# Kernel optimization log

Measured on AMD Instinct MI355X. Metric: run time of the kernel, lower is better.

Reference implementation:

```python
import jax, jax.numpy as jnp
import numpy as np

B, T, D, H = 2, 2048, 2048, 16
DK = D // H  # 128
THETA = 10000.0


def _rope_angles():
    inv_freq = 1.0 / (THETA ** (np.arange(0, DK, 2, dtype=np.float32) / DK))  # (DK/2,)
    pos = np.arange(T, dtype=np.float32)
    freqs = pos[:, None] * inv_freq[None, :]  # (T, DK/2)
    return jnp.asarray(np.broadcast_to(freqs[None], (B, T, DK // 2)).copy())


def setup_inputs() -> dict:
    key = jax.random.key(0)
    k1, k2, k3 = jax.random.split(key, 3)
    x = jax.random.normal(k1, (B, T, D), dtype=jnp.float32)
    Wqkv = jax.random.normal(k2, (D, 3 * D), dtype=jnp.float32) * (D ** -0.5)
    Wout = jax.random.normal(k3, (D, D), dtype=jnp.float32) * (D ** -0.5)
    return {"x": x, "freqs": _rope_angles(), "Wqkv": Wqkv, "Wout": Wout}


def _apply_rope(xh, cos, sin):
    # xh: (B,T,H,DK); consecutive pairs form complex numbers (torch view_as_complex)
    xr = xh[..., 0::2]  # (B,T,H,DK/2) real parts
    xi = xh[..., 1::2]  # imag parts
    # cos/sin: (B,T,1,DK/2)
    or_ = xr * cos - xi * sin
    oi_ = xr * sin + xi * cos
    return jnp.stack([or_, oi_], axis=-1).reshape(xh.shape)


def reference(x, freqs, Wqkv, Wout):
    qkv = x @ Wqkv  # (B,T,3D)
    qkv = qkv.reshape(B, T, H, 3 * DK)
    q, k, v = qkv[..., :DK], qkv[..., DK:2 * DK], qkv[..., 2 * DK:]
    cos = jnp.cos(freqs)[:, :, None, :]
    sin = jnp.sin(freqs)[:, :, None, :]
    q = _apply_rope(q, cos, sin)
    k = _apply_rope(k, cos, sin)
    # (B,H,T,DK)
    q = q.transpose(0, 2, 1, 3)
    k = k.transpose(0, 2, 1, 3)
    v = v.transpose(0, 2, 1, 3)
    scores = jnp.einsum('bhqd,bhkd->bhqk', q, k) * (DK ** -0.5)
    causal = jnp.tril(jnp.ones((T, T), dtype=bool))
    scores = jnp.where(causal[None, None], scores, -jnp.inf)
    attn = jax.nn.softmax(scores, axis=-1)
    attn = jnp.nan_to_num(attn)
    out = jnp.einsum('bhqk,bhkd->bhqd', attn, v)  # (B,H,T,DK)
    out = out.transpose(0, 2, 1, 3).reshape(B, T, D)
    return out @ Wout
```

## Files before the change

### kernel.cpp

```cpp
#include <hip/hip_runtime.h>
#include <cstdint>

#define BATCH   2
#define T_SEQ   2048
#define NH      16
#define DK      128
#define DMODEL  2048
#define NQKV    6144

using short8 = __attribute__((ext_vector_type(8))) short;
using f32x4  = __attribute__((ext_vector_type(4))) float;
using f32x16 = __attribute__((ext_vector_type(16))) float;

__device__ __forceinline__ float bf2f(unsigned short u) {
    union { float f; uint32_t i; } x; x.i = ((uint32_t)u) << 16; return x.f;
}
__device__ __forceinline__ unsigned short f2bf(float f) {
    union { float f; uint32_t i; } x; x.f = f;
    uint32_t r = x.i + 0x7fffu + ((x.i >> 16) & 1u);
    return (unsigned short)(r >> 16);
}

__device__ __forceinline__ void async_load16(const unsigned short* g, unsigned short* l) {
    __builtin_amdgcn_global_load_lds(
        (const __attribute__((address_space(1))) unsigned int*)g,
        (__attribute__((address_space(3))) unsigned int*)l,
        16, 0, 0);
}


__global__ void cast_x_kernel(const float* __restrict__ x,
                              unsigned short* __restrict__ xb, int n4) {
    int i = blockIdx.x * 256 + threadIdx.x;
    if (i >= n4) return;
    float4 v = ((const float4*)x)[i];
    ushort4 o;
    o.x = f2bf(v.x); o.y = f2bf(v.y); o.z = f2bf(v.z); o.w = f2bf(v.w);
    ((ushort4*)xb)[i] = o;
}

__global__ void wtrans_kernel(const float* __restrict__ W,
                              unsigned short* __restrict__ WT, int K, int N) {
    __shared__ unsigned short tile[64][65];
    int k0 = blockIdx.y * 64, n0 = blockIdx.x * 64;
    for (int it = 0; it < 16; ++it) {
        int idx = it * 256 + threadIdx.x;
        int r = idx >> 6, c = idx & 63;
        tile[r][c] = f2bf(W[(size_t)(k0 + r) * N + n0 + c]);
    }
    __syncthreads();
    for (int it = 0; it < 16; ++it) {
        int idx = it * 256 + threadIdx.x;
        int r = idx >> 6, c = idx & 63;
        WT[(size_t)(n0 + r) * K + k0 + c] = tile[c][r];
    }
}

template <int MODE>
__global__ __launch_bounds__(256) void gemm_bt_kernel(
    const unsigned short* __restrict__ A, const unsigned short* __restrict__ BT,
    float* __restrict__ Cout,
    unsigned short* __restrict__ qraw, unsigned short* __restrict__ kraw,
    unsigned short* __restrict__ vtb,
    int M, int N, int K) {
    __shared__ __align__(16) unsigned short As[128 * 64];
    __shared__ __align__(16) unsigned short Bs[128 * 64];
    const int tid = threadIdx.x;
    const int w = tid >> 6, lane = tid & 63;
    const int l31 = lane & 31, lhi = lane >> 5;
    const int m0 = blockIdx.y * 128, n0 = blockIdx.x * 128;
    const int wm = (w & 1) * 64, wn = (w >> 1) * 64;

    f32x16 acc[2][2];
#pragma unroll
    for (int a = 0; a < 2; ++a)
#pragma unroll
        for (int b = 0; b < 2; ++b)
#pragma unroll
            for (int r = 0; r < 16; ++r) acc[a][b][r] = 0.f;

    for (int k0 = 0; k0 < K; k0 += 64) {
#pragma unroll
        for (int j = 0; j < 4; ++j) {
            int c   = (w * 4 + j) * 64 + lane;
            int row = c >> 3;
            int kcg = (c & 7) ^ (row & 7);
            async_load16(A  + (size_t)(m0 + row) * K + k0 + kcg * 8,
                         As + (size_t)(w * 4 + j) * 64 * 8);
            async_load16(BT + (size_t)(n0 + row) * K + k0 + kcg * 8,
                         Bs + (size_t)(w * 4 + j) * 64 * 8);
        }
        __syncthreads();
#pragma unroll
        for (int ks = 0; ks < 4; ++ks) {
            short8 af[2], bfr[2];
#pragma unroll
            for (int mt = 0; mt < 2; ++mt) {
                int row = wm + mt * 32 + l31;
                int kcs = (ks * 2 + lhi) ^ (row & 7);
                af[mt] = *(const short8*)(As + row * 64 + kcs * 8);
            }
#pragma unroll
            for (int nt = 0; nt < 2; ++nt) {
                int row = wn + nt * 32 + l31;
                int kcs = (ks * 2 + lhi) ^ (row & 7);
                bfr[nt] = *(const short8*)(Bs + row * 64 + kcs * 8);
            }
#pragma unroll
            for (int mt = 0; mt < 2; ++mt)
#pragma unroll
                for (int nt = 0; nt < 2; ++nt)
                    acc[mt][nt] = __builtin_amdgcn_mfma_f32_32x32x16_bf16(
                        af[mt], bfr[nt], acc[mt][nt], 0, 0, 0);
        }
        __syncthreads();
    }

    if (MODE == 0) {
#pragma unroll
        for (int mt = 0; mt < 2; ++mt)
#pragma unroll
            for (int nt = 0; nt < 2; ++nt)
#pragma unroll
                for (int r = 0; r < 16; ++r) {
                    int row = m0 + wm + mt * 32 + (r & 3) + 8 * (r >> 2) + 4 * lhi;
                    int col = n0 + wn + nt * 32 + l31;
                    Cout[(size_t)row * N + col] = acc[mt][nt][r];
                }
    } else {
#pragma unroll
        for (int mt = 0; mt < 2; ++mt) {
            int trowb = m0 + wm + mt * 32;
            int bi = trowb >> 11;
            int tb = trowb & (T_SEQ - 1);
#pragma unroll
            for (int nt = 0; nt < 2; ++nt) {
                int colb = n0 + wn + nt * 32;
                int h    = colb / 384;
                int r3   = colb - h * 384;
                int sec  = r3 >> 7;
                int dk   = (r3 & 127) + l31;
                if (sec < 2) {
                    unsigned short* dst = (sec == 0 ? qraw : kraw) +
                        ((size_t)(bi * NH + h) * T_SEQ + tb) * DK + dk;
#pragma unroll
                    for (int r = 0; r < 16; ++r) {
                        int t = (r & 3) + 8 * (r >> 2) + 4 * lhi;
                        dst[(size_t)t * DK] = f2bf(acc[mt][nt][r]);
                    }
                } else {
                    unsigned short* dst =
                        vtb + ((size_t)(bi * NH + h) * DK + dk) * T_SEQ + tb;
#pragma unroll
                    for (int g = 0; g < 4; ++g) {
                        ushort4 p;
                        p.x = f2bf(acc[mt][nt][4 * g + 0]);
                        p.y = f2bf(acc[mt][nt][4 * g + 1]);
                        p.z = f2bf(acc[mt][nt][4 * g + 2]);
                        p.w = f2bf(acc[mt][nt][4 * g + 3]);
                        *(ushort4*)(dst + 8 * g + 4 * lhi) = p;
                    }
                }
            }
        }
    }
}

__global__ void rope_kernel(unsigned short* __restrict__ qraw,
                            unsigned short* __restrict__ kraw,
                            const float* __restrict__ freqs) {
    int linear = blockIdx.x * 256 + threadIdx.x;
    int i  = linear & 63;
    int t  = (linear >> 6) & (T_SEQ - 1);
    int bh = linear >> 17;
    int b  = bh >> 4;
    float f  = freqs[((size_t)b * T_SEQ + t) * 64 + i];
    float cs = __cosf(f), sn = __sinf(f);
    size_t off = ((size_t)bh * T_SEQ + t) * DK + 2 * i;
    ushort2 qp = *(ushort2*)(qraw + off);
    ushort2 kp = *(ushort2*)(kraw + off);
    float qr = bf2f(qp.x), qi = bf2f(qp.y);
    float kr = bf2f(kp.x), ki = bf2f(kp.y);
    ushort2 qo, ko;
    qo.x = f2bf(qr * cs - qi * sn); qo.y = f2bf(qr * sn + qi * cs);
    ko.x = f2bf(kr * cs - ki * sn); ko.y = f2bf(kr * sn + ki * cs);
    *(ushort2*)(qraw + off) = qo;
    *(ushort2*)(kraw + off) = ko;
}

__global__ __launch_bounds__(256) void attn_kernel(
    const unsigned short* __restrict__ qb, const unsigned short* __restrict__ kb,
    const unsigned short* __restrict__ vt, unsigned short* __restrict__ ctx) {
    __shared__ __align__(16) unsigned short Ks[2][64 * 128];
    __shared__ __align__(16) unsigned short Vs[2][128 * 64];
    __shared__ __align__(16) unsigned short pbuf[4][16 * 68];
    const int qt   = 31 - blockIdx.y;
    const int u    = blockIdx.x;
    const int bh   = ((u & 7) << 2) | (u >> 3);
    const int q0   = qt * 64;
    const int w    = threadIdx.x >> 6, lane = threadIdx.x & 63;
    const int lrow = lane & 15, quad = lane >> 4;
    const int qrow = q0 + w * 16;
    const float sc2 = 0.08838834764831845f * 1.4426950408889634f;
    const short8 vone = {16256, 16256, 16256, 16256, 16256, 16256, 16256, 16256};

    short8 aq[4];
    const unsigned short* qbase = qb + ((size_t)bh * T_SEQ + qrow + lrow) * DK;
#pragma unroll
    for (int kk = 0; kk < 4; ++kk)
        aq[kk] = *(const short8*)(qbase + kk * 32 + quad * 8);

    f32x4 o[8];
#pragma unroll
    for (int d = 0; d < 8; ++d) o[d] = (f32x4){0.f, 0.f, 0.f, 0.f};
    f32x4 ol = (f32x4){0.f, 0.f, 0.f, 0.f};

    const unsigned short* kg0 = kb + (size_t)bh * T_SEQ * DK;
    const unsigned short* vg0 = vt + (size_t)bh * DK * T_SEQ;

    auto stage = [&](int kt, int sbuf) {
        const unsigned short* kg = kg0 + (size_t)kt * 64 * DK;
        const unsigned short* vg = vg0 + kt * 64;
        unsigned short* Kd = &Ks[sbuf][0];
        unsigned short* Vd = &Vs[sbuf][0];
#pragma unroll
        for (int j = 0; j < 4; ++j) {
            int c = (w * 4 + j) * 64 + lane;
            int kr_ = c >> 4, kc = (c & 15) ^ (kr_ & 7);
            async_load16(kg + (size_t)kr_ * DK + kc * 8, Kd + c * 8);
            int vr = c >> 3, vc = (c & 7) ^ (vr & 7);
            async_load16(vg + (size_t)vr * T_SEQ + vc * 8, Vd + c * 8);
        }
    };

    stage(0, 0);
    for (int kt = 0; kt <= qt; ++kt) {
        __syncthreads();
        if (kt < qt) stage(kt + 1, (kt + 1) & 1);
        const unsigned short* Kb = &Ks[kt & 1][0];
        const unsigned short* Vb = &Vs[kt & 1][0];

        f32x4 s[4];
#pragma unroll
        for (int nt = 0; nt < 4; ++nt) s[nt] = (f32x4){0.f, 0.f, 0.f, 0.f};
#pragma unroll
        for (int kk = 0; kk < 4; ++kk)
#pragma unroll
            for (int nt = 0; nt < 4; ++nt) {
                int row = nt * 16 + lrow;
                int kc = (kk * 4 + quad) ^ (row & 7);
                short8 bk = *(const short8*)(Kb + row * 128 + kc * 8);
                s[nt] = __builtin_amdgcn_mfma_f32_16x16x32_bf16(aq[kk], bk, s[nt], 0, 0, 0);
            }

        const bool diag = (kt == qt);
        unsigned short* pb = &pbuf[w][0];
#pragma unroll
        for (int nt = 0; nt < 4; ++nt)
#pragma unroll
            for (int r = 0; r < 4; ++r) {
                float p = exp2f(fmaf(s[nt][r], sc2, -12.0f));
                if (diag && (nt * 16 + lrow > w * 16 + quad * 4 + r)) p = 0.f;
                pb[(quad * 4 + r) * 68 + nt * 16 + lrow] = f2bf(p);
            }
        __builtin_amdgcn_s_waitcnt(0xc07f);
        short8 ap[2];
#pragma unroll
        for (int kk2 = 0; kk2 < 2; ++kk2)
            ap[kk2] = *(const short8*)(pb + lrow * 68 + kk2 * 32 + quad * 8);

#pragma unroll
        for (int kk2 = 0; kk2 < 2; ++kk2)
            ol = __builtin_amdgcn_mfma_f32_16x16x32_bf16(ap[kk2], vone, ol, 0, 0, 0);
#pragma unroll
        for (int d = 0; d < 8; ++d)
#pragma unroll
            for (int kk2 = 0; kk2 < 2; ++kk2) {
                int row = d * 16 + lrow;
                int vc = (kk2 * 4 + quad) ^ (row & 7);
                short8 bv = *(const short8*)(Vb + row * 64 + vc * 8);
                o[d] = __builtin_amdgcn_mfma_f32_16x16x32_bf16(ap[kk2], bv, o[d], 0, 0, 0);
            }
    }

    const int b = bh >> 4, h = bh & 15;
    float rl[4];
#pragma unroll
    for (int r = 0; r < 4; ++r) rl[r] = 1.0f / ol[r];
#pragma unroll
    for (int d = 0; d < 8; ++d)
#pragma unroll
        for (int r = 0; r < 4; ++r) {
            int row = qrow + quad * 4 + r;
            ctx[((size_t)(b * T_SEQ + row)) * DMODEL + h * DK + d * 16 + lrow] =
                f2bf(o[d][r] * rl[r]);
        }
}

extern "C" void kernel_launch(void* const* d_in, const int* in_sizes, int n_in,
                              void* d_out, int out_size, void* d_ws, size_t ws_size,
                              hipStream_t stream) {
    const float* x     = (const float*)d_in[0];
    const float* freqs = (const float*)d_in[1];
    const float* Wqkv  = (const float*)d_in[2];
    const float* Wout  = (const float*)d_in[3];
    float* out = (float*)d_out;
    char* ws = (char*)d_ws;
    unsigned short* xb    = (unsigned short*)(ws);
    unsigned short* ctx   = (unsigned short*)(ws);
    unsigned short* wqkvT = (unsigned short*)(ws + 16777216);
    unsigned short* woutT = (unsigned short*)(ws + 41943040);
    unsigned short* qraw  = (unsigned short*)(ws + 50331648);
    unsigned short* kraw  = (unsigned short*)(ws + 67108864);
    unsigned short* vtb   = (unsigned short*)(ws + 83886080);

    cast_x_kernel<<<8192, 256, 0, stream>>>(x, xb, 2097152);
    wtrans_kernel<<<dim3(96, 32), 256, 0, stream>>>(Wqkv, wqkvT, DMODEL, NQKV);
    wtrans_kernel<<<dim3(32, 32), 256, 0, stream>>>(Wout, woutT, DMODEL, DMODEL);
    gemm_bt_kernel<1><<<dim3(48, 32), 256, 0, stream>>>(
        xb, wqkvT, nullptr, qraw, kraw, vtb, BATCH * T_SEQ, NQKV, DMODEL);
    rope_kernel<<<16384, 256, 0, stream>>>(qraw, kraw, freqs);
    attn_kernel<<<dim3(32, 32), 256, 0, stream>>>(qraw, kraw, vtb, ctx);
    gemm_bt_kernel<0><<<dim3(16, 32), 256, 0, stream>>>(
        ctx, woutT, out, nullptr, nullptr, nullptr, BATCH * T_SEQ, DMODEL, DMODEL);
}
```

Measured before the change: 378.2 us.

## Replace QKV GEMM with 256x256-tile 8-wave ping-pong pipelined kernel

Swaps the generic templated GEMM for the QKV projection with a dedicated kernel that uses 256x256 tiles, 512 threads and 16x16x32 MFMAs. Each K step is split into eight phases that interleave async global-to-LDS half-tile loads with MFMA work, using explicit waitcnt, barriers and setprio. The LDS layout is XOR-swizzled and blocks are remapped to improve L2 locality. The aim is to hide memory latency and raise MFMA utilisation on the largest GEMM, at the cost of heavy register use (128 accumulators) and fragile hand-tuned synchronisation.

```diff
diff --git a/kernel.cpp b/kernel.cpp
--- a/kernel.cpp
+++ b/kernel.cpp
@@ -127,40 +127,134 @@
                     int col = n0 + wn + nt * 32 + l31;
                     Cout[(size_t)row * N + col] = acc[mt][nt][r];
                 }
-    } else {
-#pragma unroll
-        for (int mt = 0; mt < 2; ++mt) {
-            int trowb = m0 + wm + mt * 32;
-            int bi = trowb >> 11;
-            int tb = trowb & (T_SEQ - 1);
-#pragma unroll
-            for (int nt = 0; nt < 2; ++nt) {
-                int colb = n0 + wn + nt * 32;
-                int h    = colb / 384;
-                int r3   = colb - h * 384;
-                int sec  = r3 >> 7;
-                int dk   = (r3 & 127) + l31;
-                if (sec < 2) {
-                    unsigned short* dst = (sec == 0 ? qraw : kraw) +
-                        ((size_t)(bi * NH + h) * T_SEQ + tb) * DK + dk;
-#pragma unroll
-                    for (int r = 0; r < 16; ++r) {
-                        int t = (r & 3) + 8 * (r >> 2) + 4 * lhi;
-                        dst[(size_t)t * DK] = f2bf(acc[mt][nt][r]);
-                    }
-                } else {
-                    unsigned short* dst =
-                        vtb + ((size_t)(bi * NH + h) * DK + dk) * T_SEQ + tb;
-#pragma unroll
-                    for (int g = 0; g < 4; ++g) {
-                        ushort4 p;
-                        p.x = f2bf(acc[mt][nt][4 * g + 0]);
-                        p.y = f2bf(acc[mt][nt][4 * g + 1]);
-                        p.z = f2bf(acc[mt][nt][4 * g + 2]);
-                        p.w = f2bf(acc[mt][nt][4 * g + 3]);
-                        *(ushort4*)(dst + 8 * g + 4 * lhi) = p;
-                    }
-                }
+    }
+}
+
+#define G1_K 2048
+#define G1_N 6144
+
+#define PHASE(BUF, QM, QN, VM, ...)                                             \
+  {                                                                             \
+    short8 paf[4][2], pbf[2][2];                                                \
+    _Pragma("unroll") for (int mt = 0; mt < 4; ++mt)                            \
+      _Pragma("unroll") for (int ks = 0; ks < 2; ++ks)                          \
+        paf[mt][ks] = *(const short8*)(&As[BUF][((wm + (QM)*64 + mt*16 + l15)   \
+            << 6) + (((ks*4 + quad) ^ l7) << 3)]);                              \
+    _Pragma("unroll") for (int nt = 0; nt < 2; ++nt)                            \
+      _Pragma("unroll") for (int ks = 0; ks < 2; ++ks)                          \
+        pbf[nt][ks] = *(const short8*)(&Bs[BUF][((wn + (QN)*32 + nt*16 + l15)   \
+            << 6) + (((ks*4 + quad) ^ l7) << 3)]);                              \
+    __VA_ARGS__;                                                                \
+    asm volatile("s_waitcnt lgkmcnt(8)" ::: "memory");                          \
+    __builtin_amdgcn_s_barrier();                                               \
+    asm volatile("s_waitcnt lgkmcnt(0)" ::: "memory");                          \
+    __builtin_amdgcn_sched_barrier(0);                                          \
+    __builtin_amdgcn_s_setprio(1);                                              \
+    _Pragma("unroll") for (int mt = 0; mt < 4; ++mt)                            \
+      _Pragma("unroll") for (int nt = 0; nt < 2; ++nt)                          \
+        _Pragma("unroll") for (int ks = 0; ks < 2; ++ks)                        \
+          acc[(QM)*4 + mt][(QN)*2 + nt] =                                       \
+              __builtin_amdgcn_mfma_f32_16x16x32_bf16(                          \
+                  paf[mt][ks], pbf[nt][ks], acc[(QM)*4 + mt][(QN)*2 + nt],      \
+                  0, 0, 0);                                                     \
+    __builtin_amdgcn_s_setprio(0);                                              \
+    VM;                                                                         \
+    __builtin_amdgcn_s_barrier();                                               \
+  }
+
+__global__ __launch_bounds__(512, 2) void gemm8p_qkv_kernel(
+    const unsigned short* __restrict__ A, const unsigned short* __restrict__ BT,
+    unsigned short* __restrict__ qraw, unsigned short* __restrict__ kraw,
+    unsigned short* __restrict__ vtb) {
+    __shared__ __align__(16) unsigned short As[2][256 * 64];
+    __shared__ __align__(16) unsigned short Bs[2][256 * 64];
+
+    const int tid = threadIdx.x;
+    const int w = tid >> 6, lane = tid & 63;
+    const int l15 = lane & 15, quad = lane >> 4, l7 = lane & 7;
+    const int wm = (w & 1) * 128, wn = (w >> 1) * 64;
+
+    const int id = blockIdx.x;
+    const int wg = (id & 7) * 48 + (id >> 3);
+    const int by = wg / 24, bx = wg - by * 24;
+    const int m0 = by * 256, n0 = bx * 256;
+
+    const int r64 = tid >> 3;
+    const int csw = (tid & 7) ^ (r64 & 7);
+
+    auto stageA = [&](int buf, int kt, int h) {
+#pragma unroll
+        for (int j = 0; j < 2; ++j) {
+            const int rg = h * 64 + j * 128 + r64;
+            async_load16(A + (size_t)(m0 + rg) * G1_K + kt * 64 + csw * 8,
+                         &As[buf][(h * 64 + j * 128 + w * 8) << 6]);
+        }
+    };
+    auto stageB = [&](int buf, int kt, int h) {
+#pragma unroll
+        for (int j = 0; j < 2; ++j) {
+            const int rbw = j * 128 + ((w >> 2) << 6) + h * 32 + ((w & 3) << 3);
+            const int rg  = rbw + (lane >> 3);
+            async_load16(BT + (size_t)(n0 + rg) * G1_K + kt * 64 + csw * 8,
+                         &Bs[buf][rbw << 6]);
+        }
+    };
+
+    f32x4 acc[8][4];
+#pragma unroll
+    for (int i = 0; i < 8; ++i)
+#pragma unroll
+        for (int j = 0; j < 4; ++j) acc[i][j] = (f32x4){0.f, 0.f, 0.f, 0.f};
+
+    stageA(0, 0, 0); stageB(0, 0, 0); stageA(0, 0, 1); stageB(0, 0, 1);
+    stageA(1, 1, 0); stageB(1, 1, 0);
+    asm volatile("s_waitcnt vmcnt(4)" ::: "memory");
+    __builtin_amdgcn_s_barrier();
+
+    const int NI = G1_K / 128;
+    for (int it = 0; it < NI; ++it) {
+        const int t1 = 2 * it + 1;
+        const bool last = (it == NI - 1);
+        PHASE(0, 0, 0, (void)0, stageA(1, t1, 1))
+        PHASE(0, 0, 1, (void)0, stageB(1, t1, 1))
+        PHASE(0, 1, 0, (void)0, if (!last) stageA(0, t1 + 1, 0))
+        PHASE(0, 1, 1,
+              if (last) { asm volatile("s_waitcnt vmcnt(0)" ::: "memory"); }
+              else      { asm volatile("s_waitcnt vmcnt(4)" ::: "memory"); },
+              if (!last) stageB(0, t1 + 1, 0))
+        PHASE(1, 0, 0, (void)0, if (!last) stageA(0, t1 + 1, 1))
+        PHASE(1, 0, 1, (void)0, if (!last) stageB(0, t1 + 1, 1))
+        PHASE(1, 1, 0, (void)0, if (!last) stageA(1, t1 + 2, 0))
+        PHASE(1, 1, 1,
+              if (!last) { asm volatile("s_waitcnt vmcnt(4)" ::: "memory"); },
+              if (!last) stageB(1, t1 + 2, 0))
+    }
+
+#pragma unroll
+    for (int i8 = 0; i8 < 8; ++i8) {
+        const int grow0 = m0 + wm + i8 * 16 + quad * 4;
+        const int bi = grow0 >> 11;
+        const int tb = grow0 & (T_SEQ - 1);
+#pragma unroll
+        for (int j4 = 0; j4 < 4; ++j4) {
+            const int gcol = n0 + wn + j4 * 16 + l15;
+            const int h   = gcol / 384;
+            const int r3  = gcol - h * 384;
+            const int sec = r3 >> 7;
+            const int dk  = r3 & 127;
+            if (sec < 2) {
+                unsigned short* dst = (sec == 0 ? qraw : kraw) +
+                    ((size_t)(bi * NH + h) * T_SEQ + tb) * DK + dk;
+#pragma unroll
+                for (int r = 0; r < 4; ++r)
+                    dst[(size_t)r * DK] = f2bf(acc[i8][j4][r]);
+            } else {
+                unsigned short* dst = vtb +
+                    ((size_t)(bi * NH + h) * DK + dk) * T_SEQ + tb;
+                ushort4 p;
+                p.x = f2bf(acc[i8][j4][0]); p.y = f2bf(acc[i8][j4][1]);
+                p.z = f2bf(acc[i8][j4][2]); p.w = f2bf(acc[i8][j4][3]);
+                *(ushort4*)dst = p;
             }
         }
     }
@@ -317,8 +411,7 @@
     cast_x_kernel<<<8192, 256, 0, stream>>>(x, xb, 2097152);
     wtrans_kernel<<<dim3(96, 32), 256, 0, stream>>>(Wqkv, wqkvT, DMODEL, NQKV);
     wtrans_kernel<<<dim3(32, 32), 256, 0, stream>>>(Wout, woutT, DMODEL, DMODEL);
-    gemm_bt_kernel<1><<<dim3(48, 32), 256, 0, stream>>>(
-        xb, wqkvT, nullptr, qraw, kraw, vtb, BATCH * T_SEQ, NQKV, DMODEL);
+    gemm8p_qkv_kernel<<<384, 512, 0, stream>>>(xb, wqkvT, qraw, kraw, vtb);
     rope_kernel<<<16384, 256, 0, stream>>>(qraw, kraw, freqs);
     attn_kernel<<<dim3(32, 32), 256, 0, stream>>>(qraw, kraw, vtb, ctx);
     gemm_bt_kernel<0><<<dim3(16, 32), 256, 0, stream>>>(
```

New measurement: 407.3 us. +7.7%, slower.
